# Performance work log

Measured on AMD Instinct MI355X. Metric: run time of the kernel, lower is better.

## Reference

```python
import jax, jax.numpy as jnp
import numpy as np

# TT config (matches init_kwargs)
NUM_TABLES = 4
P = (100, 100, 100)          # tt_p_shapes, prod = num_embeddings = 1e6
Q = (4, 4, 4)                # tt_q_shapes, prod = embedding_dim = 64
R = (1, 32, 32, 1)           # tt_ranks with boundary ranks
BAGS_PER_TABLE = 8192
POOL = 16                    # indices per bag


def setup_inputs() -> dict:
    key = jax.random.key(0)
    k1, k2, k3, k4 = jax.random.split(key, 4)
    nnz = NUM_TABLES * BAGS_PER_TABLE * POOL      # 524288
    B = NUM_TABLES * BAGS_PER_TABLE               # 32768 bags total
    indices = jax.random.randint(k1, (nnz,), 0, P[0] * P[1] * P[2], dtype=jnp.int64)
    offsets = (jnp.arange(B + 1, dtype=jnp.int64) * POOL)
    scale = 0.05  # small init, akin to approx-normal weight_dist
    tt_core_0 = jax.random.normal(k2, (NUM_TABLES, P[0], R[0] * Q[0] * R[1]), dtype=jnp.float32) * scale
    tt_core_1 = jax.random.normal(k3, (NUM_TABLES, P[1], R[1] * Q[1] * R[2]), dtype=jnp.float32) * scale
    tt_core_2 = jax.random.normal(k4, (NUM_TABLES, P[2], R[2] * Q[2] * R[3]), dtype=jnp.float32) * scale
    return {"indices": indices, "offsets": offsets,
            "tt_core_0": tt_core_0, "tt_core_1": tt_core_1, "tt_core_2": tt_core_2}


def reference(indices, offsets, tt_core_0, tt_core_1, tt_core_2):
    nnz = indices.shape[0]
    B = offsets.shape[0] - 1
    bags_per_table = B // NUM_TABLES

    # bag id for each nonzero (embedding-bag semantics), then table id per nonzero
    rowidx = jnp.searchsorted(offsets, jnp.arange(nnz, dtype=offsets.dtype), side='right') - 1
    tableidx = rowidx // bags_per_table

    # decompose flat row index into TT indices (C-order over p-shapes,
    # matching tt_matrix_to_full row layout)
    i0 = indices // (P[1] * P[2])
    i1 = (indices // P[2]) % P[1]
    i2 = indices % P[2]

    # gather per-lookup core slices
    c0 = tt_core_0[tableidx, i0].reshape(nnz, Q[0], R[1])          # r0 == 1
    c1 = tt_core_1[tableidx, i1].reshape(nnz, R[1], Q[1], R[2])
    c2 = tt_core_2[tableidx, i2].reshape(nnz, R[2], Q[2])          # r3 == 1

    # on-the-fly TT contraction to reconstruct embedding rows [nnz, D]
    t = jnp.einsum('nar,nrbs->nabs', c0, c1)                       # [nnz, q0, q1, r2]
    rows = jnp.einsum('nabs,nsc->nabc', t, c2).reshape(nnz, Q[0] * Q[1] * Q[2])

    # sum-pool per bag
    out = jax.ops.segment_sum(rows, rowidx, num_segments=B)        # [B, D]
    return out
```

## Files before the change

### kernel.cpp

```cpp
#include <hip/hip_runtime.h>
#include <stdint.h>

#define NT 4
#define PP 100
#define TT_BYTES (4ull * 100 * 100 * 1024)


__device__ __forceinline__ uint32_t f2bf(float f) {
    union { float f; uint32_t u; } v; v.f = f;
    uint32_t u = v.u;
    return (u + 0x7fffu + ((u >> 16) & 1u)) >> 16;
}

__device__ __forceinline__ float dot2bf(uint32_t a, uint32_t b, float c) {
    float d;
    asm("v_dot2_f32_bf16 %0, %1, %2, %3" : "=v"(d) : "v"(a), "v"(b), "v"(c));
    return d;
}

__global__ __launch_bounds__(256)
void c2pack_kernel(const float* __restrict__ c2g, uint32_t* __restrict__ c2p) {
    int t = blockIdx.x * 256 + threadIdx.x;
    if (t >= NT * PP * 64) return;
    int c = t & 3, sg = (t >> 2) & 15, rest = t >> 6;
    int i2 = rest % PP, tab = rest / PP;
    const float* src = c2g + (size_t)(tab * PP + i2) * 128;
    float e = src[(2 * sg) * 4 + c];
    float o = src[(2 * sg + 1) * 4 + c];
    c2p[t] = f2bf(e) | (f2bf(o) << 16);
}

__global__ __launch_bounds__(128, 3)
void tt_phase1(const float* __restrict__ c0g, const float* __restrict__ c1g,
               unsigned short* __restrict__ tT) {
    __shared__ float c1s[32 * 128];
    __shared__ float c0t[16 * 132];

    int blk = blockIdx.x;
    int tab   = blk / 700;
    int rem   = blk % 700;
    int i1    = rem / 7;
    int chunk = rem % 7;
    int i0_base = chunk * 16;
    int tid = threadIdx.x;

    const float4* c1p = (const float4*)(c1g + (size_t)(tab * PP + i1) * 4096);
    float4* c1v = (float4*)c1s;
    #pragma unroll
    for (int it = 0; it < 8; ++it) c1v[tid + 128 * it] = c1p[tid + 128 * it];

    #pragma unroll
    for (int it = 0; it < 16; ++it) {
        int f = tid + 128 * it;
        int i0l = f >> 7;
        int x   = f & 127;
        int a = x >> 5, r = x & 31;
        int i0 = i0_base + i0l; if (i0 > PP - 1) i0 = PP - 1;
        c0t[i0l * 132 + r * 4 + a] = c0g[(size_t)(tab * PP + i0) * 128 + x];
    }
    __syncthreads();

    int u  = tid >> 4;
    int sg = tid & 15;

    float acc[2][2][16];
    #pragma unroll
    for (int ii = 0; ii < 2; ++ii)
        #pragma unroll
        for (int e = 0; e < 2; ++e)
            #pragma unroll
            for (int q = 0; q < 16; ++q) acc[ii][e][q] = 0.f;

    #pragma unroll 4
    for (int r = 0; r < 32; ++r) {
        float4 av0 = *(const float4*)&c0t[(2 * u) * 132 + r * 4];
        float4 av1 = *(const float4*)&c0t[(2 * u + 1) * 132 + r * 4];
        const float* a0 = (const float*)&av0;
        const float* a1 = (const float*)&av1;
        #pragma unroll
        for (int b = 0; b < 4; ++b) {
            float2 bv = *(const float2*)&c1s[r * 128 + b * 32 + 2 * sg];
            #pragma unroll
            for (int a = 0; a < 4; ++a) {
                acc[0][0][a * 4 + b] += a0[a] * bv.x;
                acc[0][1][a * 4 + b] += a0[a] * bv.y;
                acc[1][0][a * 4 + b] += a1[a] * bv.x;
                acc[1][1][a * 4 + b] += a1[a] * bv.y;
            }
        }
    }

    #pragma unroll
    for (int ii = 0; ii < 2; ++ii) {
        int i0 = i0_base + 2 * u + ii;
        if (i0 >= PP) continue;
        size_t combo = (size_t)tab * 10000 + (size_t)i0 * 100 + (size_t)i1;
        char* base = (char*)tT + combo * 1024 + (size_t)sg * 64;
        #pragma unroll
        for (int k = 0; k < 4; ++k) {
            uint4 w;
            w.x = f2bf(acc[ii][0][4*k+0]) | (f2bf(acc[ii][1][4*k+0]) << 16);
            w.y = f2bf(acc[ii][0][4*k+1]) | (f2bf(acc[ii][1][4*k+1]) << 16);
            w.z = f2bf(acc[ii][0][4*k+2]) | (f2bf(acc[ii][1][4*k+2]) << 16);
            w.w = f2bf(acc[ii][0][4*k+3]) | (f2bf(acc[ii][1][4*k+3]) << 16);
            *(uint4*)(base + k * 16) = w;
        }
    }
}

__global__ __launch_bounds__(256, 3)
void tt_phase2(const int* __restrict__ indices, const int* __restrict__ offsets,
               const unsigned short* __restrict__ tT, const uint32_t* __restrict__ c2p,
               float* __restrict__ out, int bags_per_table, int B) {
    int lane = threadIdx.x & 63;
    int wv   = threadIdx.x >> 6;
    int bag  = blockIdx.x * 4 + wv;
    if (bag >= B) return;
    int sub = lane >> 4;
    int sg  = lane & 15;
    int tab = bag / bags_per_table;
    int start = offsets[bag];

    const uint4* c2q = (const uint4*)c2p;

    const uint4* tp[4];
    int ci[4];
    #pragma unroll
    for (int j = 0; j < 4; ++j) {
        uint32_t idx = (uint32_t)indices[start + j * 4 + sub];
        uint32_t i0 = idx / 10000u;
        uint32_t r1 = idx - i0 * 10000u;
        uint32_t i1 = r1 / 100u;
        uint32_t i2 = r1 - i1 * 100u;
        tp[j] = (const uint4*)((const char*)tT +
                 ((size_t)tab * 10000u + i0 * 100u + i1) * 1024 + (size_t)sg * 64);
        ci[j] = (tab * PP + (int)i2) * 16 + sg;
    }

    uint4 T[4][4];
    uint4 C[4];
    #pragma unroll
    for (int j = 0; j < 4; ++j) {
        T[j][0] = tp[j][0]; T[j][1] = tp[j][1];
        T[j][2] = tp[j][2]; T[j][3] = tp[j][3];
        C[j] = c2q[ci[j]];
    }

    float acc[64];
    #pragma unroll
    for (int d = 0; d < 64; ++d) acc[d] = 0.f;

    #pragma unroll
    for (int j = 0; j < 4; ++j) {
        uint32_t cd[4] = { C[j].x, C[j].y, C[j].z, C[j].w };
        #pragma unroll
        for (int k = 0; k < 4; ++k) {
            uint32_t td[4] = { T[j][k].x, T[j][k].y, T[j][k].z, T[j][k].w };
            #pragma unroll
            for (int m = 0; m < 4; ++m) {
                int d0 = (4 * k + m) * 4;
                acc[d0 + 0] = dot2bf(td[m], cd[0], acc[d0 + 0]);
                acc[d0 + 1] = dot2bf(td[m], cd[1], acc[d0 + 1]);
                acc[d0 + 2] = dot2bf(td[m], cd[2], acc[d0 + 2]);
                acc[d0 + 3] = dot2bf(td[m], cd[3], acc[d0 + 3]);
            }
        }
    }

    #pragma unroll
    for (int m = 32; m >= 1; m >>= 1) {
        bool up = (lane & m) != 0;
        #pragma unroll
        for (int j = 0; j < m; ++j) {
            float lo = acc[j], hi = acc[j + m];
            float send = up ? lo : hi;
            float recv = __shfl_xor(send, m, 64);
            acc[j] = (up ? hi : lo) + recv;
        }
    }
    out[(size_t)bag * 64 + lane] = acc[0];
}

extern "C" void kernel_launch(void* const* d_in, const int* in_sizes, int n_in,
                              void* d_out, int out_size, void* d_ws, size_t ws_size,
                              hipStream_t stream) {
    const int*   indices = (const int*)d_in[0];
    const int*   offsets = (const int*)d_in[1];
    const float* c0      = (const float*)d_in[2];
    const float* c1      = (const float*)d_in[3];
    const float* c2      = (const float*)d_in[4];
    float* out = (float*)d_out;

    int B = in_sizes[1] - 1;
    int bags_per_table = B / NT;

    unsigned short* tT  = (unsigned short*)d_ws;
    uint32_t*       c2p = (uint32_t*)((char*)d_ws + TT_BYTES);

    c2pack_kernel<<<dim3((NT * PP * 64 + 255) / 256), dim3(256), 0, stream>>>(c2, c2p);
    tt_phase1<<<dim3(NT * PP * 7), dim3(128), 0, stream>>>(c0, c1, tT);
    tt_phase2<<<dim3((B + 3) / 4), dim3(256), 0, stream>>>(indices, offsets, tT, c2p, out,
                                                           bags_per_table, B);
}
```

Measured before the change: 155.1 us.

## Use MFMA bf16 16x16x32 for phase-2 contraction with XCD-aware bag mapping

Measured after the change: 182.6 us. 17.7% more time.

```diff
diff --git a/kernel.cpp b/kernel.cpp
--- a/kernel.cpp
+++ b/kernel.cpp
@@ -6,28 +6,25 @@
 #define TT_BYTES (4ull * 100 * 100 * 1024)
 
 
+typedef __attribute__((ext_vector_type(8))) short short8;
+typedef __attribute__((ext_vector_type(4))) float floatx4;
+union U4S8 { uint4 u; short8 s; };
+
 __device__ __forceinline__ uint32_t f2bf(float f) {
     union { float f; uint32_t u; } v; v.f = f;
     uint32_t u = v.u;
     return (u + 0x7fffu + ((u >> 16) & 1u)) >> 16;
 }
 
-__device__ __forceinline__ float dot2bf(uint32_t a, uint32_t b, float c) {
-    float d;
-    asm("v_dot2_f32_bf16 %0, %1, %2, %3" : "=v"(d) : "v"(a), "v"(b), "v"(c));
-    return d;
-}
-
 __global__ __launch_bounds__(256)
-void c2pack_kernel(const float* __restrict__ c2g, uint32_t* __restrict__ c2p) {
+void c2pack_kernel(const float* __restrict__ c2g, uint32_t* __restrict__ c2a) {
     int t = blockIdx.x * 256 + threadIdx.x;
     if (t >= NT * PP * 64) return;
-    int c = t & 3, sg = (t >> 2) & 15, rest = t >> 6;
+    int jp = t & 3, sgrp = (t >> 2) & 3, n = (t >> 4) & 3, rest = t >> 6;
     int i2 = rest % PP, tab = rest / PP;
     const float* src = c2g + (size_t)(tab * PP + i2) * 128;
-    float e = src[(2 * sg) * 4 + c];
-    float o = src[(2 * sg + 1) * 4 + c];
-    c2p[t] = f2bf(e) | (f2bf(o) << 16);
+    int s = sgrp * 8 + 2 * jp;
+    c2a[t] = f2bf(src[s * 4 + n]) | (f2bf(src[(s + 1) * 4 + n]) << 16);
 }
 
 __global__ __launch_bounds__(128, 3)
@@ -95,90 +92,73 @@
         int i0 = i0_base + 2 * u + ii;
         if (i0 >= PP) continue;
         size_t combo = (size_t)tab * 10000 + (size_t)i0 * 100 + (size_t)i1;
-        char* base = (char*)tT + combo * 1024 + (size_t)sg * 64;
+        uint32_t* bp = (uint32_t*)((char*)tT + combo * 1024) + sg;
         #pragma unroll
-        for (int k = 0; k < 4; ++k) {
-            uint4 w;
-            w.x = f2bf(acc[ii][0][4*k+0]) | (f2bf(acc[ii][1][4*k+0]) << 16);
-            w.y = f2bf(acc[ii][0][4*k+1]) | (f2bf(acc[ii][1][4*k+1]) << 16);
-            w.z = f2bf(acc[ii][0][4*k+2]) | (f2bf(acc[ii][1][4*k+2]) << 16);
-            w.w = f2bf(acc[ii][0][4*k+3]) | (f2bf(acc[ii][1][4*k+3]) << 16);
-            *(uint4*)(base + k * 16) = w;
-        }
+        for (int ab = 0; ab < 16; ++ab)
+            bp[ab * 16] = f2bf(acc[ii][0][ab]) | (f2bf(acc[ii][1][ab]) << 16);
     }
 }
 
-__global__ __launch_bounds__(256, 3)
+__global__ __launch_bounds__(256, 4)
 void tt_phase2(const int* __restrict__ indices, const int* __restrict__ offsets,
-               const unsigned short* __restrict__ tT, const uint32_t* __restrict__ c2p,
+               const unsigned short* __restrict__ tT, const uint32_t* __restrict__ c2a,
                float* __restrict__ out, int bags_per_table, int B) {
     int lane = threadIdx.x & 63;
     int wv   = threadIdx.x >> 6;
-    int bag  = blockIdx.x * 4 + wv;
+    int blk  = blockIdx.x;
+
+    int tab, bag;
+    if (((gridDim.x & 7) == 0) && ((B & 31) == 0)) {
+        int xcd = blk & 7;
+        tab = xcd >> 1;
+        int within = ((blk >> 3) << 1) + (xcd & 1);
+        bag = tab * bags_per_table + within * 4 + wv;
+    } else {
+        bag = blk * 4 + wv;
+        tab = bag / bags_per_table;
+    }
     if (bag >= B) return;
-    int sub = lane >> 4;
-    int sg  = lane & 15;
-    int tab = bag / bags_per_table;
+
+    int n = lane & 15, quad = lane >> 4;
+    int laneoff = n * 64 + quad * 16;
+
     int start = offsets[bag];
+    uint32_t idx = (uint32_t)indices[start + n];
+    uint32_t i0 = idx / 10000u;
+    uint32_t r1 = idx - i0 * 10000u;
+    uint32_t i1 = r1 / 100u;
+    uint32_t i2 = r1 - i1 * 100u;
+    uint32_t code = (i0 * 100u + i1) * 128u + i2;
 
-    const uint4* c2q = (const uint4*)c2p;
+    const char* tbase = (const char*)tT + (size_t)tab * 10000u * 1024u + laneoff;
+    const char* cbase = (const char*)c2a + (size_t)tab * PP * 256u + laneoff;
+    bool bact = (n < 4);
 
-    const uint4* tp[4];
-    int ci[4];
+    uint32_t codes[16];
+    uint4 af[16];
     #pragma unroll
-    for (int j = 0; j < 4; ++j) {
-        uint32_t idx = (uint32_t)indices[start + j * 4 + sub];
-        uint32_t i0 = idx / 10000u;
-        uint32_t r1 = idx - i0 * 10000u;
-        uint32_t i1 = r1 / 100u;
-        uint32_t i2 = r1 - i1 * 100u;
-        tp[j] = (const uint4*)((const char*)tT +
-                 ((size_t)tab * 10000u + i0 * 100u + i1) * 1024 + (size_t)sg * 64);
-        ci[j] = (tab * PP + (int)i2) * 16 + sg;
+    for (int j = 0; j < 16; ++j) {
+        uint32_t cj = __shfl((int)code, j, 64);
+        codes[j] = cj;
+        af[j] = *(const uint4*)(tbase + (size_t)(cj >> 7) * 1024u);
     }
 
-    uint4 T[4][4];
-    uint4 C[4];
+    floatx4 acc = {0.f, 0.f, 0.f, 0.f};
+    uint4 zero4 = make_uint4(0u, 0u, 0u, 0u);
     #pragma unroll
-    for (int j = 0; j < 4; ++j) {
-        T[j][0] = tp[j][0]; T[j][1] = tp[j][1];
-        T[j][2] = tp[j][2]; T[j][3] = tp[j][3];
-        C[j] = c2q[ci[j]];
+    for (int j = 0; j < 16; ++j) {
+        uint4 bu = bact ? *(const uint4*)(cbase + (size_t)(codes[j] & 127u) * 256u) : zero4;
+        U4S8 a, b; a.u = af[j]; b.u = bu;
+        acc = __builtin_amdgcn_mfma_f32_16x16x32_bf16(a.s, b.s, acc, 0, 0, 0);
     }
 
-    float acc[64];
-    #pragma unroll
-    for (int d = 0; d < 64; ++d) acc[d] = 0.f;
-
-    #pragma unroll
-    for (int j = 0; j < 4; ++j) {
-        uint32_t cd[4] = { C[j].x, C[j].y, C[j].z, C[j].w };
-        #pragma unroll
-        for (int k = 0; k < 4; ++k) {
-            uint32_t td[4] = { T[j][k].x, T[j][k].y, T[j][k].z, T[j][k].w };
-            #pragma unroll
-            for (int m = 0; m < 4; ++m) {
-                int d0 = (4 * k + m) * 4;
-                acc[d0 + 0] = dot2bf(td[m], cd[0], acc[d0 + 0]);
-                acc[d0 + 1] = dot2bf(td[m], cd[1], acc[d0 + 1]);
-                acc[d0 + 2] = dot2bf(td[m], cd[2], acc[d0 + 2]);
-                acc[d0 + 3] = dot2bf(td[m], cd[3], acc[d0 + 3]);
-            }
-        }
+    if (bact) {
+        float* op = out + (size_t)bag * 64 + quad * 16 + n;
+        op[0]  = acc[0];
+        op[4]  = acc[1];
+        op[8]  = acc[2];
+        op[12] = acc[3];
     }
-
-    #pragma unroll
-    for (int m = 32; m >= 1; m >>= 1) {
-        bool up = (lane & m) != 0;
-        #pragma unroll
-        for (int j = 0; j < m; ++j) {
-            float lo = acc[j], hi = acc[j + m];
-            float send = up ? lo : hi;
-            float recv = __shfl_xor(send, m, 64);
-            acc[j] = (up ? hi : lo) + recv;
-        }
-    }
-    out[(size_t)bag * 64 + lane] = acc[0];
 }
 
 extern "C" void kernel_launch(void* const* d_in, const int* in_sizes, int n_in,
@@ -195,10 +175,10 @@
     int bags_per_table = B / NT;
 
     unsigned short* tT  = (unsigned short*)d_ws;
-    uint32_t*       c2p = (uint32_t*)((char*)d_ws + TT_BYTES);
+    uint32_t*       c2a = (uint32_t*)((char*)d_ws + TT_BYTES);
 
-    c2pack_kernel<<<dim3((NT * PP * 64 + 255) / 256), dim3(256), 0, stream>>>(c2, c2p);
+    c2pack_kernel<<<dim3((NT * PP * 64 + 255) / 256), dim3(256), 0, stream>>>(c2, c2a);
     tt_phase1<<<dim3(NT * PP * 7), dim3(128), 0, stream>>>(c0, c1, tT);
-    tt_phase2<<<dim3((B + 3) / 4), dim3(256), 0, stream>>>(indices, offsets, tT, c2p, out,
+    tt_phase2<<<dim3((B + 3) / 4), dim3(256), 0, stream>>>(indices, offsets, tT, c2a, out,
                                                            bags_per_table, B);
 }
```
